# Kernel tuning notes

Measured on AMD Instinct MI355X. Metric: run time of the kernel, lower is better.

## Reference

```python
import jax, jax.numpy as jnp
import numpy as np

D_MODEL = 512
HEADS = 8
D_FF = 1024
EPS = 1e-5


def layer_norm(x, gamma, beta):
    mu = jnp.mean(x, axis=-1, keepdims=True)
    var = jnp.mean(jnp.square(x - mu), axis=-1, keepdims=True)
    return (x - mu) * jax.lax.rsqrt(var + EPS) * gamma + beta


def mha(q, k, v, mask=None):
    # q,k,v: [B, S, D]; no input/output projections in the original module
    B, Sq, D = q.shape
    Sk = k.shape[1]
    dk = D // HEADS
    qh = q.reshape(B, Sq, HEADS, dk).transpose(0, 2, 1, 3)  # [B,H,Sq,dk]
    kh = k.reshape(B, Sk, HEADS, dk).transpose(0, 2, 1, 3)
    vh = v.reshape(B, Sk, HEADS, dk).transpose(0, 2, 1, 3)
    scores = jnp.einsum('bhqd,bhkd->bhqk', qh, kh) / np.sqrt(dk).astype(q.dtype)
    if mask is not None:
        scores = jnp.where(mask == 0, jnp.asarray(-1e9, scores.dtype), scores)
    attn = jax.nn.softmax(scores, axis=-1)  # dropout is identity in eval mode
    out = jnp.einsum('bhqk,bhkd->bhqd', attn, vh)
    return out.transpose(0, 2, 1, 3).reshape(B, Sq, D)


def setup_inputs() -> dict:
    key = jax.random.key(0)
    ks = jax.random.split(key, 8)
    B, S = 4, 2048
    x = jax.random.normal(ks[0], (B, S, D_MODEL), dtype=jnp.float32)
    encoder_output = jax.random.normal(ks[1], (B, S, D_MODEL), dtype=jnp.float32)
    mask = jax.random.randint(ks[2], (B, 1, S, S), 0, 2, dtype=jnp.int32)
    params = {
        'ln1_g': jnp.ones((D_MODEL,), jnp.float32), 'ln1_b': jnp.zeros((D_MODEL,), jnp.float32),
        'ln2_g': jnp.ones((D_MODEL,), jnp.float32), 'ln2_b': jnp.zeros((D_MODEL,), jnp.float32),
        'ln3_g': jnp.ones((D_MODEL,), jnp.float32), 'ln3_b': jnp.zeros((D_MODEL,), jnp.float32),
        'W1': jax.random.normal(ks[3], (D_MODEL, D_FF), jnp.float32) * (1.0 / np.sqrt(D_MODEL)),
        'b1': jnp.zeros((D_FF,), jnp.float32),
        'W2': jax.random.normal(ks[4], (D_FF, D_MODEL), jnp.float32) * (1.0 / np.sqrt(D_FF)),
        'b2': jnp.zeros((D_MODEL,), jnp.float32),
    }
    return {'x': x, 'encoder_output': encoder_output, 'mask': mask, **params}


def reference(x, encoder_output, mask, ln1_g, ln1_b, ln2_g, ln2_b, ln3_g, ln3_b, W1, b1, W2, b2):
    # pre-norm masked self-attention + residual (dropout = identity, eval mode)
    x1 = layer_norm(x, ln1_g, ln1_b)
    x = x + mha(x1, x1, x1, mask)
    # pre-norm cross-attention + residual
    x1 = layer_norm(x, ln2_g, ln2_b)
    x = x + mha(x1, encoder_output, encoder_output, None)
    # pre-norm FFN + residual
    x1 = layer_norm(x, ln3_g, ln3_b)
    h = jax.nn.relu(x1 @ W1 + b1)
    x = x + (h @ W2 + b2)
    return x
```

## Files before the change

kernel.cpp:

```cpp
#include <hip/hip_runtime.h>
#include <hip/hip_bf16.h>

#define D_MODEL 512
#define HEADS   8
#define DK      64
#define D_FF    1024
#define SEQ     2048
#define BATCH   4
#define NTOK    (BATCH*SEQ)
#define NELEM   (NTOK*D_MODEL)

#define QSCALE  0.18033688011112042f
#define MFIX    40.0f

typedef __attribute__((ext_vector_type(8))) short bf8_t;
typedef __attribute__((ext_vector_type(4))) float f4_t;

#define GLD16(gp, lp) __builtin_amdgcn_global_load_lds( \
    (const __attribute__((address_space(1))) void*)(gp), \
    (__attribute__((address_space(3))) void*)(lp), 16, 0, 0)

__device__ __forceinline__ float ldf(const void* p, size_t i, int f32) {
    return f32 ? ((const float*)p)[i] : __bfloat162float(((const __hip_bfloat16*)p)[i]);
}
__device__ __forceinline__ short f2bf(float f) {
    union { __hip_bfloat16 h; short s; } u; u.h = __float2bfloat16(f); return u.s;
}
__device__ __forceinline__ float bf2f(short s) {
    return __uint_as_float(((unsigned)(unsigned short)s) << 16);
}
__device__ __forceinline__ unsigned fbits(float f) { return __float_as_uint(f); }

__device__ __forceinline__ float fast_exp2(float x) {
    float r; asm("v_exp_f32 %0, %1" : "=v"(r) : "v"(x)); return r;
}

__global__ void detect_k(const uint4* __restrict__ w, int* __restrict__ flags) {
    __shared__ int found;
    if (threadIdx.x == 0) found = 0;
    __syncthreads();
    int hit = 0;
    for (int i = threadIdx.x; i < 4096; i += 256) {
        uint4 u = w[i];
        if (((u.x & 0x7F80u) == 0x7F80u) || ((u.y & 0x7F80u) == 0x7F80u) ||
            ((u.z & 0x7F80u) == 0x7F80u) || ((u.w & 0x7F80u) == 0x7F80u)) hit = 1;
    }
    if (hit) atomicOr(&found, 1);
    __syncthreads();
    if (threadIdx.x == 0) flags[0] = found ? 1 : 0;
}

__device__ __forceinline__ void transpose_body(const void* src, __hip_bfloat16* dst,
                                               int K, int N, int bxi, int byi, int f32,
                                               __hip_bfloat16 (*t)[33]) {
    int bx = bxi * 32, by = byi * 32;
    int tx = threadIdx.x & 31, ty = threadIdx.x >> 5;
    #pragma unroll
    for (int j = 0; j < 32; j += 8)
        t[ty + j][tx] = __float2bfloat16(ldf(src, (size_t)(by + ty + j) * N + bx + tx, f32));
    __syncthreads();
    #pragma unroll
    for (int j = 0; j < 32; j += 8)
        dst[(size_t)(bx + ty + j) * K + by + tx] = t[tx][ty + j];
}

__global__ __launch_bounds__(256)
void prep_k(const void* __restrict__ enc, const int* __restrict__ mask,
            const void* __restrict__ W1, const void* __restrict__ W2,
            const void* __restrict__ x, const void* __restrict__ ln1g,
            const void* __restrict__ ln1b,
            const int* __restrict__ flagp,
            __hip_bfloat16* __restrict__ bufE, unsigned* __restrict__ mb,
            __hip_bfloat16* __restrict__ W1T, __hip_bfloat16* __restrict__ W2T,
            float* __restrict__ bufX, __hip_bfloat16* __restrict__ bufQ) {
    __shared__ __hip_bfloat16 t[32][33];
    int f32 = *flagp;
    int bid = blockIdx.x;
    if (bid < 16384) {
        int i = bid * 256 + threadIdx.x;
        bufE[i] = __float2bfloat16(ldf(enc, i, f32));
    } else if (bid < 18432) {
        int row  = (bid - 16384) * 4 + (threadIdx.x >> 6);
        int lane = threadIdx.x & 63;
        const int* mr = mask + (size_t)row * SEQ;
        for (int it = 0; it < SEQ/64; it++) {
            unsigned long long bal = __ballot(mr[it*64 + lane] != 0);
            if (lane == 0)  mb[(size_t)row*(SEQ/32) + it*2]     = (unsigned)bal;
            if (lane == 32) mb[(size_t)row*(SEQ/32) + it*2 + 1] = (unsigned)(bal >> 32);
        }
    } else if (bid < 18944) {
        int lb = bid - 18432;
        transpose_body(W1, W1T, D_MODEL, D_FF, lb & 31, lb >> 5, f32, t);
    } else if (bid < 19456) {
        int lb = bid - 18944;
        transpose_body(W2, W2T, D_FF, D_MODEL, lb & 15, lb >> 4, f32, t);
    } else {
        int row  = (bid - 19456) * 4 + (threadIdx.x >> 6);
        int lane = threadIdx.x & 63;
        size_t base = (size_t)row * D_MODEL;
        float v[8];
        float s = 0.f;
        #pragma unroll
        for (int i = 0; i < 8; i++) { v[i] = ldf(x, base + lane + i*64, f32); s += v[i]; }
        #pragma unroll
        for (int off = 32; off; off >>= 1) s += __shfl_xor(s, off);
        float mu = s * (1.f / D_MODEL);
        float ss = 0.f;
        #pragma unroll
        for (int i = 0; i < 8; i++) { float d = v[i] - mu; ss += d * d; }
        #pragma unroll
        for (int off = 32; off; off >>= 1) ss += __shfl_xor(ss, off);
        float rstd = rsqrtf(ss * (1.f / D_MODEL) + 1e-5f);
        #pragma unroll
        for (int i = 0; i < 8; i++) {
            int c = lane + i*64;
            bufX[base + c] = v[i];
            bufQ[base + c] = __float2bfloat16((v[i] - mu) * rstd * ldf(ln1g, c, f32) + ldf(ln1b, c, f32));
        }
    }
}

__global__ __launch_bounds__(256)
void layernorm_k(const float* __restrict__ x, const void* __restrict__ g,
                 const void* __restrict__ b, const int* __restrict__ flagp,
                 __hip_bfloat16* __restrict__ y) {
    int f32  = *flagp;
    int row  = blockIdx.x * 4 + (threadIdx.x >> 6);
    int lane = threadIdx.x & 63;
    const float* xr = x + (size_t)row * D_MODEL;
    float v[8];
    float s = 0.f;
    #pragma unroll
    for (int i = 0; i < 8; i++) { v[i] = xr[lane + i*64]; s += v[i]; }
    #pragma unroll
    for (int off = 32; off; off >>= 1) s += __shfl_xor(s, off);
    float mu = s * (1.f / D_MODEL);
    float ss = 0.f;
    #pragma unroll
    for (int i = 0; i < 8; i++) { float d = v[i] - mu; ss += d * d; }
    #pragma unroll
    for (int off = 32; off; off >>= 1) ss += __shfl_xor(ss, off);
    float rstd = rsqrtf(ss * (1.f / D_MODEL) + 1e-5f);
    __hip_bfloat16* yr = y + (size_t)row * D_MODEL;
    #pragma unroll
    for (int i = 0; i < 8; i++) {
        int c = lane + i*64;
        yr[c] = __float2bfloat16((v[i] - mu) * rstd * ldf(g, c, f32) + ldf(b, c, f32));
    }
}

__device__ __forceinline__ bf8_t prescale_q(bf8_t q) {
    bf8_t r;
    #pragma unroll
    for (int j = 0; j < 8; j++) r[j] = f2bf(bf2f(q[j]) * QSCALE);
    return r;
}

template<bool HAS_MASK>
__global__ __launch_bounds__(256, 2)
void attn_mfma_k(const __hip_bfloat16* __restrict__ Q, const __hip_bfloat16* __restrict__ K,
                 const __hip_bfloat16* __restrict__ V, const unsigned* __restrict__ mbits,
                 float* __restrict__ Xout) {
    int bid0 = blockIdx.x;
    int bid = ((bid0 & 7) << 6) | (bid0 >> 3);
    int qt = bid & 15;
    int h  = (bid >> 4) & 7;
    int b  = bid >> 7;
    int q0 = qt * 128;
    int tid  = threadIdx.x;
    int w    = tid >> 6;
    int lane = tid & 63;
    int c    = lane & 15;
    int quad = lane >> 4;

    __shared__ __hip_bfloat16 Kt[4][64 * 64];
    __shared__ __hip_bfloat16 VT[4][64 * 64];
    __shared__ __hip_bfloat16 Pb[4][2][16 * 64];

    bf8_t qf[2][2];
    #pragma unroll
    for (int g = 0; g < 2; g++) {
        const __hip_bfloat16* qrp = Q + ((size_t)(b*SEQ + q0 + 32*w + 16*g + c)) * D_MODEL + h*DK;
        qf[g][0] = prescale_q(*(const bf8_t*)(qrp + quad*8));
        qf[g][1] = prescale_q(*(const bf8_t*)(qrp + 32 + quad*8));
    }

    int kpo[4][2], vpo[4][2];
    #pragma unroll
    for (int t = 0; t < 4; t++)
        #pragma unroll
        for (int kh = 0; kh < 2; kh++) {
            int row = 16*t + c;
            kpo[t][kh] = (row*64 + (((4*kh + quad) ^ (row & 7)) * 8)) * 2;
            vpo[t][kh] = (row*64 + (((4*kh + quad) ^ (row & 7) ^ ((row >> 3) & 7)) * 8)) * 2;
        }

    int key0 = (tid >> 3) * 2, d0 = (tid & 7) * 8;
    int vtwo[8];
    #pragma unroll
    for (int j = 0; j < 8; j++) {
        int dk = d0 + j;
        int ch = (key0 >> 3) ^ (dk & 7) ^ ((dk >> 3) & 7);
        vtwo[j] = dk*128 + ch*16 + (key0 & 7)*2;
    }

    int krow[2], kc8[2];
    #pragma unroll
    for (int i = 0; i < 2; i++) {
        int idx = i*256 + tid;
        krow[i] = idx >> 3;
        kc8[i]  = ((idx & 7) ^ (krow[i] & 7)) * 8;
    }

    char* pbw[2] = { (char*)&Pb[w][0][0], (char*)&Pb[w][1][0] };
    int pwoff[4], proff[2];
    #pragma unroll
    for (int nt = 0; nt < 4; nt++)
        pwoff[nt] = c*128 + (((2*nt + (quad >> 1)) ^ (c & 7)) * 16) + (quad & 1)*8;
    #pragma unroll
    for (int kh = 0; kh < 2; kh++)
        proff[kh] = c*128 + (((4*kh + quad) ^ (c & 7)) * 16);

    const unsigned* mrp[2] = {nullptr, nullptr};
    if (HAS_MASK) {
        mrp[0] = mbits + (size_t)(b*SEQ + q0 + 32*w + c) * (SEQ/32);
        mrp[1] = mrp[0] + (size_t)16 * (SEQ/32);
    }
    int qsh = quad * 4;

    short onev = (c == 0) ? (short)0x3F80 : (short)0;
    bf8_t ones = {onev, onev, onev, onev, onev, onev, onev, onev};

    f4_t o[2][4];
    #pragma unroll
    for (int g = 0; g < 2; g++)
        #pragma unroll
        for (int mt = 0; mt < 4; mt++) o[g][mt] = (f4_t){0.f,0.f,0.f,0.f};
    f4_t l_acc[2] = {(f4_t){0.f,0.f,0.f,0.f}, (f4_t){0.f,0.f,0.f,0.f}};

    const size_t kvbase = (size_t)b * SEQ * D_MODEL + (size_t)h * DK;

    auto loadV = [&](int k0, bf8_t (&r0)[2], bf8_t (&r1)[2]) {
        #pragma unroll
        for (int t = 0; t < 2; t++) {
            const __hip_bfloat16* Vg = V + kvbase + (size_t)(k0 + t*64 + key0) * D_MODEL + d0;
            r0[t] = *(const bf8_t*)Vg;
            r1[t] = *(const bf8_t*)(Vg + D_MODEL);
        }
    };
    auto stageK = [&](int k0, int bufbase) {
        #pragma unroll
        for (int t = 0; t < 2; t++) {
            const __hip_bfloat16* Kg = K + kvbase + (size_t)(k0 + t*64) * D_MODEL;
            GLD16(Kg + (size_t)krow[0]*D_MODEL + kc8[0], (char*)&Kt[bufbase + t][0] + (w*64) * 16);
            GLD16(Kg + (size_t)krow[1]*D_MODEL + kc8[1], (char*)&Kt[bufbase + t][0] + (256 + w*64) * 16);
        }
    };
    auto writeV = [&](const bf8_t (&r0)[2], const bf8_t (&r1)[2], int bufbase) {
        #pragma unroll
        for (int t = 0; t < 2; t++) {
            const unsigned* v0u = (const unsigned*)&r0[t];
            const unsigned* v1u = (const unsigned*)&r1[t];
            char* vb = (char*)&VT[bufbase + t][0];
            #pragma unroll
            for (int dw = 0; dw < 4; dw++) {
                *(unsigned*)(vb + vtwo[2*dw])     = __builtin_amdgcn_perm(v1u[dw], v0u[dw], 0x05040100u);
                *(unsigned*)(vb + vtwo[2*dw + 1]) = __builtin_amdgcn_perm(v1u[dw], v0u[dw], 0x07060302u);
            }
        }
    };

    uint4 pm[2];
    if (HAS_MASK) { pm[0] = *(const uint4*)(mrp[0]); pm[1] = *(const uint4*)(mrp[1]); }
    bf8_t cv0[2], cv1[2];
    loadV(0, cv0, cv1);
    stageK(0, 0);
    writeV(cv0, cv1, 0);
    __syncthreads();

    for (int ph = 0; ph < SEQ/128; ph++) {
        int pb = (ph & 1) ? 2 : 0;
        int nb = pb ^ 2;

        uint4 nm[2];
        bf8_t nv0[2], nv1[2];
        if (ph < SEQ/128 - 1) {
            int kn = (ph + 1) * 128;
            if (HAS_MASK) {
                nm[0] = *(const uint4*)(mrp[0] + (kn >> 5));
                nm[1] = *(const uint4*)(mrp[1] + (kn >> 5));
            }
            loadV(kn, nv0, nv1);
            stageK(kn, nb);
        }

        #pragma unroll
        for (int t = 0; t < 2; t++) {
            const char* ktb = (const char*)&Kt[pb + t][0];
            const char* vtb = (const char*)&VT[pb + t][0];

            f4_t s[2][4];
            #pragma unroll
            for (int nt = 0; nt < 4; nt++) {
                s[0][nt] = (f4_t){-MFIX,-MFIX,-MFIX,-MFIX};
                s[1][nt] = (f4_t){-MFIX,-MFIX,-MFIX,-MFIX};
            }
            __builtin_amdgcn_s_setprio(1);
            #pragma unroll
            for (int nt = 0; nt < 4; nt++)
                #pragma unroll
                for (int kh = 0; kh < 2; kh++) {
                    bf8_t kf = *(const bf8_t*)(ktb + kpo[nt][kh]);
                    s[0][nt] = __builtin_amdgcn_mfma_f32_16x16x32_bf16(kf, qf[0][kh], s[0][nt], 0, 0, 0);
                    s[1][nt] = __builtin_amdgcn_mfma_f32_16x16x32_bf16(kf, qf[1][kh], s[1][nt], 0, 0, 0);
                }
            __builtin_amdgcn_s_setprio(0);

            #pragma unroll
            for (int g = 0; g < 2; g++) {
                unsigned wq0 = 0xffffffffu, wq1 = 0xffffffffu;
                if (HAS_MASK) {
                    wq0 = (t ? pm[g].z : pm[g].x) >> qsh;
                    wq1 = (t ? pm[g].w : pm[g].y) >> qsh;
                }
                #pragma unroll
                for (int nt = 0; nt < 4; nt++) {
                    #pragma unroll
                    for (int r = 0; r < 4; r++) {
                        float p = fast_exp2(s[g][nt][r]);
                        if (HAS_MASK) {
                            unsigned sel = (nt < 2) ? wq0 : wq1;
                            if (!((sel >> ((nt & 1)*16 + r)) & 1u)) p = 0.f;
                        }
                        s[g][nt][r] = p;
                    }
                    unsigned pk0 = __builtin_amdgcn_perm(fbits(s[g][nt][1]), fbits(s[g][nt][0]), 0x07060302u);
                    unsigned pk1 = __builtin_amdgcn_perm(fbits(s[g][nt][3]), fbits(s[g][nt][2]), 0x07060302u);
                    *(uint2*)(pbw[g] + pwoff[nt]) = make_uint2(pk0, pk1);
                }
            }

            __builtin_amdgcn_s_setprio(1);
            #pragma unroll
            for (int kh = 0; kh < 2; kh++) {
                bf8_t pfA = *(const bf8_t*)(pbw[0] + proff[kh]);
                bf8_t pfB = *(const bf8_t*)(pbw[1] + proff[kh]);
                l_acc[0] = __builtin_amdgcn_mfma_f32_16x16x32_bf16(ones, pfA, l_acc[0], 0, 0, 0);
                l_acc[1] = __builtin_amdgcn_mfma_f32_16x16x32_bf16(ones, pfB, l_acc[1], 0, 0, 0);
                #pragma unroll
                for (int mt = 0; mt < 4; mt++) {
                    bf8_t vf = *(const bf8_t*)(vtb + vpo[mt][kh]);
                    o[0][mt] = __builtin_amdgcn_mfma_f32_16x16x32_bf16(vf, pfA, o[0][mt], 0, 0, 0);
                    o[1][mt] = __builtin_amdgcn_mfma_f32_16x16x32_bf16(vf, pfB, o[1][mt], 0, 0, 0);
                }
            }
            __builtin_amdgcn_s_setprio(0);
        }

        if (ph < SEQ/128 - 1) {
            writeV(nv0, nv1, nb);
            if (HAS_MASK) { pm[0] = nm[0]; pm[1] = nm[1]; }
        }
        __syncthreads();
    }

    #pragma unroll
    for (int g = 0; g < 2; g++) {
        float lq = __shfl(l_acc[g][0], c);
        float il = 1.f / fmaxf(lq, 1e-35f);
        size_t rb = ((size_t)(b*SEQ + q0 + 32*w + 16*g + c)) * D_MODEL + h*DK;
        #pragma unroll
        for (int mt = 0; mt < 4; mt++) {
            float4* xp = (float4*)(Xout + rb + 16*mt + quad*4);
            float4 x4 = *xp;
            x4.x += o[g][mt][0] * il;
            x4.y += o[g][mt][1] * il;
            x4.z += o[g][mt][2] * il;
            x4.w += o[g][mt][3] * il;
            *xp = x4;
        }
    }
}

__global__ __launch_bounds__(256, 2)
void gemm_relu_k(const __hip_bfloat16* __restrict__ A, const __hip_bfloat16* __restrict__ BT,
                 const void* __restrict__ bias, const int* __restrict__ flagp,
                 __hip_bfloat16* __restrict__ C, int Ksz, int Nsz) {
    int f32 = *flagp;
    __shared__ __hip_bfloat16 As[2][128 * 64];
    __shared__ __hip_bfloat16 Bs[2][128 * 64];
    int tid  = threadIdx.x;
    int w    = tid >> 6;
    int c    = tid & 15;
    int quad = (tid >> 4) & 3;
    int wy = w >> 1, wx = w & 1;
    int lin = blockIdx.y * gridDim.x + blockIdx.x;
    int swz = ((lin & 7) << 6) | (lin >> 3);
    int r0 = (swz >> 3) * 128, c0 = (swz & 7) * 128;

    f4_t acc[4][4];
    #pragma unroll
    for (int i = 0; i < 4; i++)
        #pragma unroll
        for (int j = 0; j < 4; j++) acc[i][j] = (f4_t){0.f,0.f,0.f,0.f};

    auto stage = [&](int k0, int bi) {
        #pragma unroll
        for (int i = 0; i < 4; i++) {
            int idx = i*256 + tid;
            int row = idx >> 3, c8 = idx & 7;
            GLD16(A  + (size_t)(r0 + row) * Ksz + k0 + ((c8 ^ (row & 7)) * 8),
                  (char*)&As[bi][0] + (size_t)(i*256 + w*64) * 16);
            GLD16(BT + (size_t)(c0 + row) * Ksz + k0 + ((c8 ^ (row & 7)) * 8),
                  (char*)&Bs[bi][0] + (size_t)(i*256 + w*64) * 16);
        }
    };

    stage(0, 0);
    __syncthreads();
    int nk = Ksz >> 6;
    for (int ks = 0; ks < nk; ks++) {
        int bi = ks & 1;
        if (ks + 1 < nk) stage((ks + 1) << 6, bi ^ 1);

        #pragma unroll
        for (int kh = 0; kh < 2; kh++) {
            bf8_t af[4], bf[4];
            #pragma unroll
            for (int mt = 0; mt < 4; mt++) {
                int row = wy*64 + mt*16 + c;
                af[mt] = *(const bf8_t*)&As[bi][row*64 + (((kh*4 + quad) ^ (row & 7)) * 8)];
            }
            #pragma unroll
            for (int nt = 0; nt < 4; nt++) {
                int row = wx*64 + nt*16 + c;
                bf[nt] = *(const bf8_t*)&Bs[bi][row*64 + (((kh*4 + quad) ^ (row & 7)) * 8)];
            }
            #pragma unroll
            for (int mt = 0; mt < 4; mt++)
                #pragma unroll
                for (int nt = 0; nt < 4; nt++)
                    acc[mt][nt] = __builtin_amdgcn_mfma_f32_16x16x32_bf16(af[mt], bf[nt], acc[mt][nt], 0, 0, 0);
        }
        __syncthreads();
    }

    #pragma unroll
    for (int mt = 0; mt < 4; mt++)
        #pragma unroll
        for (int nt = 0; nt < 4; nt++) {
            int col = c0 + wx*64 + nt*16 + c;
            float bv = ldf(bias, col, f32);
            #pragma unroll
            for (int r = 0; r < 4; r++) {
                int m = r0 + wy*64 + mt*16 + quad*4 + r;
                C[(size_t)m * Nsz + col] = __float2bfloat16(fmaxf(acc[mt][nt][r] + bv, 0.f));
            }
        }
}

__global__ __launch_bounds__(256, 2)
void gemm_out_k(const __hip_bfloat16* __restrict__ A, const __hip_bfloat16* __restrict__ BT,
                const void* __restrict__ bias, const float* __restrict__ resid,
                const int* __restrict__ flagp, void* __restrict__ out, int Ksz, int Nsz) {
    int f32 = *flagp;
    __shared__ __hip_bfloat16 As[2][128 * 64];
    __shared__ __hip_bfloat16 Bs[2][64 * 64];
    int tid  = threadIdx.x;
    int w    = tid >> 6;
    int c    = tid & 15;
    int quad = (tid >> 4) & 3;
    int lin = blockIdx.y * gridDim.x + blockIdx.x;
    int swz = ((lin & 7) << 6) | (lin >> 3);
    int r0 = (swz >> 3) * 128, c0 = (swz & 7) * 64;

    f4_t acc[2][4];
    #pragma unroll
    for (int i = 0; i < 2; i++)
        #pragma unroll
        for (int j = 0; j < 4; j++) acc[i][j] = (f4_t){0.f,0.f,0.f,0.f};

    auto stage = [&](int k0, int bi) {
        #pragma unroll
        for (int i = 0; i < 4; i++) {
            int idx = i*256 + tid;
            int row = idx >> 3, c8 = idx & 7;
            GLD16(A + (size_t)(r0 + row) * Ksz + k0 + ((c8 ^ (row & 7)) * 8),
                  (char*)&As[bi][0] + (size_t)(i*256 + w*64) * 16);
        }
        #pragma unroll
        for (int i = 0; i < 2; i++) {
            int idx = i*256 + tid;
            int row = idx >> 3, c8 = idx & 7;
            GLD16(BT + (size_t)(c0 + row) * Ksz + k0 + ((c8 ^ (row & 7)) * 8),
                  (char*)&Bs[bi][0] + (size_t)(i*256 + w*64) * 16);
        }
    };

    stage(0, 0);
    __syncthreads();
    int nk = Ksz >> 6;
    for (int ks = 0; ks < nk; ks++) {
        int bi = ks & 1;
        if (ks + 1 < nk) stage((ks + 1) << 6, bi ^ 1);

        #pragma unroll
        for (int kh = 0; kh < 2; kh++) {
            bf8_t af[2], bf[4];
            #pragma unroll
            for (int mt = 0; mt < 2; mt++) {
                int row = w*32 + mt*16 + c;
                af[mt] = *(const bf8_t*)&As[bi][row*64 + (((kh*4 + quad) ^ (row & 7)) * 8)];
            }
            #pragma unroll
            for (int nt = 0; nt < 4; nt++) {
                int row = nt*16 + c;
                bf[nt] = *(const bf8_t*)&Bs[bi][row*64 + (((kh*4 + quad) ^ (row & 7)) * 8)];
            }
            #pragma unroll
            for (int mt = 0; mt < 2; mt++)
                #pragma unroll
                for (int nt = 0; nt < 4; nt++)
                    acc[mt][nt] = __builtin_amdgcn_mfma_f32_16x16x32_bf16(af[mt], bf[nt], acc[mt][nt], 0, 0, 0);
        }
        __syncthreads();
    }

    #pragma unroll
    for (int mt = 0; mt < 2; mt++)
        #pragma unroll
        for (int nt = 0; nt < 4; nt++) {
            int col = c0 + nt*16 + c;
            float bv = ldf(bias, col, f32);
            #pragma unroll
            for (int r = 0; r < 4; r++) {
                int m = r0 + w*32 + mt*16 + quad*4 + r;
                float v = acc[mt][nt][r] + bv + resid[(size_t)m * Nsz + col];
                if (f32) ((float*)out)[(size_t)m * Nsz + col] = v;
                else     ((__hip_bfloat16*)out)[(size_t)m * Nsz + col] = __float2bfloat16(v);
            }
        }
}

extern "C" void kernel_launch(void* const* d_in, const int* in_sizes, int n_in,
                              void* d_out, int out_size, void* d_ws, size_t ws_size,
                              hipStream_t stream) {
    const void* x    = d_in[0];
    const void* enc  = d_in[1];
    const int*  mask = (const int*)d_in[2];
    const void* ln1g = d_in[3];
    const void* ln1b = d_in[4];
    const void* ln2g = d_in[5];
    const void* ln2b = d_in[6];
    const void* ln3g = d_in[7];
    const void* ln3b = d_in[8];
    const void* W1   = d_in[9];
    const void* b1   = d_in[10];
    const void* W2   = d_in[11];
    const void* b2   = d_in[12];

    char* ws = (char*)d_ws;
    float*          bufX  = (float*)ws;
    __hip_bfloat16* bufQ  = (__hip_bfloat16*)(ws + (16u<<20));
    __hip_bfloat16* bufE  = (__hip_bfloat16*)(ws + (24u<<20));
    __hip_bfloat16* bufH  = (__hip_bfloat16*)(ws + (32u<<20));
    __hip_bfloat16* W1T   = (__hip_bfloat16*)(ws + (48u<<20));
    __hip_bfloat16* W2T   = (__hip_bfloat16*)(ws + (49u<<20));
    unsigned*       mbits = (unsigned*)(ws + (50u<<20));
    int*            flags = (int*)(ws + (52u<<20));

    dim3 blk(256);
    detect_k<<<1, blk, 0, stream>>>((const uint4*)x, flags);
    prep_k<<<21504, blk, 0, stream>>>(enc, mask, W1, W2, x, ln1g, ln1b, flags,
                                      bufE, mbits, W1T, W2T, bufX, bufQ);

    attn_mfma_k<true><<<BATCH*HEADS*(SEQ/128), blk, 0, stream>>>(bufQ, bufQ, bufQ, mbits, bufX);
    layernorm_k<<<NTOK/4, blk, 0, stream>>>(bufX, ln2g, ln2b, flags, bufQ);
    attn_mfma_k<false><<<BATCH*HEADS*(SEQ/128), blk, 0, stream>>>(bufQ, bufE, bufE, nullptr, bufX);
    layernorm_k<<<NTOK/4, blk, 0, stream>>>(bufX, ln3g, ln3b, flags, bufQ);
    gemm_relu_k<<<dim3(D_FF/128, NTOK/128), blk, 0, stream>>>(bufQ, W1T, b1, flags, bufH, D_MODEL, D_FF);
    gemm_out_k<<<dim3(D_MODEL/64, NTOK/128), blk, 0, stream>>>(bufH, W2T, b2, bufX, flags, d_out, D_FF, D_MODEL);
}
```

Baseline: 330.3 us.

## Vectorize prep and layernorm I/O, shrink attention K/V tiles for higher occupancy

The prep kernel's encoder bf16 conversion and the LN1 path now read and write 8 contiguous elements per thread with float4/bf8 vectors, cutting the block count. The layernorm kernel uses the same vectorized row layout. The attention kernel stages one 64-key tile per phase instead of two, halving its K/V shared memory so launch bounds can request 3 blocks per CU. The trade is twice as many loop iterations and barriers in attention, and possibly more register pressure under the tighter bound.

```diff
diff --git a/kernel.cpp b/kernel.cpp
--- a/kernel.cpp
+++ b/kernel.cpp
@@ -76,11 +76,20 @@
     __shared__ __hip_bfloat16 t[32][33];
     int f32 = *flagp;
     int bid = blockIdx.x;
-    if (bid < 16384) {
-        int i = bid * 256 + threadIdx.x;
-        bufE[i] = __float2bfloat16(ldf(enc, i, f32));
-    } else if (bid < 18432) {
-        int row  = (bid - 16384) * 4 + (threadIdx.x >> 6);
+    if (bid < 2048) {
+        size_t i0 = ((size_t)bid * 256 + threadIdx.x) * 8;
+        bf8_t o8;
+        if (f32) {
+            const float4* ep = (const float4*)((const float*)enc + i0);
+            float4 a = ep[0], b4 = ep[1];
+            o8[0]=f2bf(a.x);  o8[1]=f2bf(a.y);  o8[2]=f2bf(a.z);  o8[3]=f2bf(a.w);
+            o8[4]=f2bf(b4.x); o8[5]=f2bf(b4.y); o8[6]=f2bf(b4.z); o8[7]=f2bf(b4.w);
+        } else {
+            o8 = *(const bf8_t*)((const __hip_bfloat16*)enc + i0);
+        }
+        *(bf8_t*)(bufE + i0) = o8;
+    } else if (bid < 4096) {
+        int row  = (bid - 2048) * 4 + (threadIdx.x >> 6);
         int lane = threadIdx.x & 63;
         const int* mr = mask + (size_t)row * SEQ;
         for (int it = 0; it < SEQ/64; it++) {
@@ -88,20 +97,31 @@
             if (lane == 0)  mb[(size_t)row*(SEQ/32) + it*2]     = (unsigned)bal;
             if (lane == 32) mb[(size_t)row*(SEQ/32) + it*2 + 1] = (unsigned)(bal >> 32);
         }
-    } else if (bid < 18944) {
-        int lb = bid - 18432;
+    } else if (bid < 4608) {
+        int lb = bid - 4096;
         transpose_body(W1, W1T, D_MODEL, D_FF, lb & 31, lb >> 5, f32, t);
-    } else if (bid < 19456) {
-        int lb = bid - 18944;
+    } else if (bid < 5120) {
+        int lb = bid - 4608;
         transpose_body(W2, W2T, D_FF, D_MODEL, lb & 15, lb >> 4, f32, t);
     } else {
-        int row  = (bid - 19456) * 4 + (threadIdx.x >> 6);
+        int row  = (bid - 5120) * 4 + (threadIdx.x >> 6);
         int lane = threadIdx.x & 63;
+        int c0   = lane * 8;
         size_t base = (size_t)row * D_MODEL;
         float v[8];
+        if (f32) {
+            const float4* xp = (const float4*)((const float*)x + base + c0);
+            float4 a = xp[0], b4 = xp[1];
+            v[0]=a.x; v[1]=a.y; v[2]=a.z; v[3]=a.w;
+            v[4]=b4.x; v[5]=b4.y; v[6]=b4.z; v[7]=b4.w;
+        } else {
+            bf8_t x8 = *(const bf8_t*)((const __hip_bfloat16*)x + base + c0);
+            #pragma unroll
+            for (int j = 0; j < 8; j++) v[j] = bf2f(x8[j]);
+        }
         float s = 0.f;
         #pragma unroll
-        for (int i = 0; i < 8; i++) { v[i] = ldf(x, base + lane + i*64, f32); s += v[i]; }
+        for (int i = 0; i < 8; i++) s += v[i];
         #pragma unroll
         for (int off = 32; off; off >>= 1) s += __shfl_xor(s, off);
         float mu = s * (1.f / D_MODEL);
@@ -111,12 +131,13 @@
         #pragma unroll
         for (int off = 32; off; off >>= 1) ss += __shfl_xor(ss, off);
         float rstd = rsqrtf(ss * (1.f / D_MODEL) + 1e-5f);
-        #pragma unroll
-        for (int i = 0; i < 8; i++) {
-            int c = lane + i*64;
-            bufX[base + c] = v[i];
-            bufQ[base + c] = __float2bfloat16((v[i] - mu) * rstd * ldf(ln1g, c, f32) + ldf(ln1b, c, f32));
-        }
+        *(float4*)(bufX + base + c0)     = make_float4(v[0], v[1], v[2], v[3]);
+        *(float4*)(bufX + base + c0 + 4) = make_float4(v[4], v[5], v[6], v[7]);
+        bf8_t q8;
+        #pragma unroll
+        for (int j = 0; j < 8; j++)
+            q8[j] = f2bf((v[j] - mu) * rstd * ldf(ln1g, c0 + j, f32) + ldf(ln1b, c0 + j, f32));
+        *(bf8_t*)(bufQ + base + c0) = q8;
     }
 }
 
@@ -127,11 +148,14 @@
     int f32  = *flagp;
     int row  = blockIdx.x * 4 + (threadIdx.x >> 6);
     int lane = threadIdx.x & 63;
+    int c0   = lane * 8;
     const float* xr = x + (size_t)row * D_MODEL;
-    float v[8];
+    const float4* xp = (const float4*)(xr + c0);
+    float4 a = xp[0], b4 = xp[1];
+    float v[8] = {a.x, a.y, a.z, a.w, b4.x, b4.y, b4.z, b4.w};
     float s = 0.f;
     #pragma unroll
-    for (int i = 0; i < 8; i++) { v[i] = xr[lane + i*64]; s += v[i]; }
+    for (int i = 0; i < 8; i++) s += v[i];
     #pragma unroll
     for (int off = 32; off; off >>= 1) s += __shfl_xor(s, off);
     float mu = s * (1.f / D_MODEL);
@@ -141,12 +165,11 @@
     #pragma unroll
     for (int off = 32; off; off >>= 1) ss += __shfl_xor(ss, off);
     float rstd = rsqrtf(ss * (1.f / D_MODEL) + 1e-5f);
-    __hip_bfloat16* yr = y + (size_t)row * D_MODEL;
-    #pragma unroll
-    for (int i = 0; i < 8; i++) {
-        int c = lane + i*64;
-        yr[c] = __float2bfloat16((v[i] - mu) * rstd * ldf(g, c, f32) + ldf(b, c, f32));
-    }
+    bf8_t y8;
+    #pragma unroll
+    for (int j = 0; j < 8; j++)
+        y8[j] = f2bf((v[j] - mu) * rstd * ldf(g, c0 + j, f32) + ldf(b, c0 + j, f32));
+    *(bf8_t*)(y + (size_t)row * D_MODEL + c0) = y8;
 }
 
 __device__ __forceinline__ bf8_t prescale_q(bf8_t q) {
@@ -157,7 +180,7 @@
 }
 
 template<bool HAS_MASK>
-__global__ __launch_bounds__(256, 2)
+__global__ __launch_bounds__(256, 3)
 void attn_mfma_k(const __hip_bfloat16* __restrict__ Q, const __hip_bfloat16* __restrict__ K,
                  const __hip_bfloat16* __restrict__ V, const unsigned* __restrict__ mbits,
                  float* __restrict__ Xout) {
@@ -173,8 +196,8 @@
     int c    = lane & 15;
     int quad = lane >> 4;
 
-    __shared__ __hip_bfloat16 Kt[4][64 * 64];
-    __shared__ __hip_bfloat16 VT[4][64 * 64];
+    __shared__ __hip_bfloat16 Kt[2][64 * 64];
+    __shared__ __hip_bfloat16 VT[2][64 * 64];
     __shared__ __hip_bfloat16 Pb[4][2][16 * 64];
 
     bf8_t qf[2][2];
@@ -240,64 +263,54 @@
 
     const size_t kvbase = (size_t)b * SEQ * D_MODEL + (size_t)h * DK;
 
-    auto loadV = [&](int k0, bf8_t (&r0)[2], bf8_t (&r1)[2]) {
-        #pragma unroll
-        for (int t = 0; t < 2; t++) {
-            const __hip_bfloat16* Vg = V + kvbase + (size_t)(k0 + t*64 + key0) * D_MODEL + d0;
-            r0[t] = *(const bf8_t*)Vg;
-            r1[t] = *(const bf8_t*)(Vg + D_MODEL);
-        }
+    auto loadV = [&](int k0, bf8_t& r0, bf8_t& r1) {
+        const __hip_bfloat16* Vg = V + kvbase + (size_t)(k0 + key0) * D_MODEL + d0;
+        r0 = *(const bf8_t*)Vg;
+        r1 = *(const bf8_t*)(Vg + D_MODEL);
     };
-    auto stageK = [&](int k0, int bufbase) {
-        #pragma unroll
-        for (int t = 0; t < 2; t++) {
-            const __hip_bfloat16* Kg = K + kvbase + (size_t)(k0 + t*64) * D_MODEL;
-            GLD16(Kg + (size_t)krow[0]*D_MODEL + kc8[0], (char*)&Kt[bufbase + t][0] + (w*64) * 16);
-            GLD16(Kg + (size_t)krow[1]*D_MODEL + kc8[1], (char*)&Kt[bufbase + t][0] + (256 + w*64) * 16);
-        }
+    auto stageK = [&](int k0, int bi) {
+        const __hip_bfloat16* Kg = K + kvbase + (size_t)k0 * D_MODEL;
+        GLD16(Kg + (size_t)krow[0]*D_MODEL + kc8[0], (char*)&Kt[bi][0] + (w*64) * 16);
+        GLD16(Kg + (size_t)krow[1]*D_MODEL + kc8[1], (char*)&Kt[bi][0] + (256 + w*64) * 16);
     };
-    auto writeV = [&](const bf8_t (&r0)[2], const bf8_t (&r1)[2], int bufbase) {
-        #pragma unroll
-        for (int t = 0; t < 2; t++) {
-            const unsigned* v0u = (const unsigned*)&r0[t];
-            const unsigned* v1u = (const unsigned*)&r1[t];
-            char* vb = (char*)&VT[bufbase + t][0];
-            #pragma unroll
-            for (int dw = 0; dw < 4; dw++) {
-                *(unsigned*)(vb + vtwo[2*dw])     = __builtin_amdgcn_perm(v1u[dw], v0u[dw], 0x05040100u);
-                *(unsigned*)(vb + vtwo[2*dw + 1]) = __builtin_amdgcn_perm(v1u[dw], v0u[dw], 0x07060302u);
-            }
+    auto writeV = [&](const bf8_t& r0, const bf8_t& r1, int bi) {
+        const unsigned* v0u = (const unsigned*)&r0;
+        const unsigned* v1u = (const unsigned*)&r1;
+        char* vb = (char*)&VT[bi][0];
+        #pragma unroll
+        for (int dw = 0; dw < 4; dw++) {
+            *(unsigned*)(vb + vtwo[2*dw])     = __builtin_amdgcn_perm(v1u[dw], v0u[dw], 0x05040100u);
+            *(unsigned*)(vb + vtwo[2*dw + 1]) = __builtin_amdgcn_perm(v1u[dw], v0u[dw], 0x07060302u);
         }
     };
 
-    uint4 pm[2];
-    if (HAS_MASK) { pm[0] = *(const uint4*)(mrp[0]); pm[1] = *(const uint4*)(mrp[1]); }
-    bf8_t cv0[2], cv1[2];
+    uint2 pm[2];
+    if (HAS_MASK) { pm[0] = *(const uint2*)(mrp[0]); pm[1] = *(const uint2*)(mrp[1]); }
+    bf8_t cv0, cv1;
     loadV(0, cv0, cv1);
     stageK(0, 0);
     writeV(cv0, cv1, 0);
     __syncthreads();
 
-    for (int ph = 0; ph < SEQ/128; ph++) {
-        int pb = (ph & 1) ? 2 : 0;
-        int nb = pb ^ 2;
-
-        uint4 nm[2];
-        bf8_t nv0[2], nv1[2];
-        if (ph < SEQ/128 - 1) {
-            int kn = (ph + 1) * 128;
+    for (int ph = 0; ph < SEQ/64; ph++) {
+        int bi = ph & 1;
+        int ni = bi ^ 1;
+
+        uint2 nm[2];
+        bf8_t nv0, nv1;
+        if (ph < SEQ/64 - 1) {
+            int kn = (ph + 1) * 64;
             if (HAS_MASK) {
-                nm[0] = *(const uint4*)(mrp[0] + (kn >> 5));
-                nm[1] = *(const uint4*)(mrp[1] + (kn >> 5));
+                nm[0] = *(const uint2*)(mrp[0] + (kn >> 5));
+                nm[1] = *(const uint2*)(mrp[1] + (kn >> 5));
             }
             loadV(kn, nv0, nv1);
-            stageK(kn, nb);
-        }
-
-        #pragma unroll
-        for (int t = 0; t < 2; t++) {
-            const char* ktb = (const char*)&Kt[pb + t][0];
-            const char* vtb = (const char*)&VT[pb + t][0];
+            stageK(kn, ni);
+        }
+
+        {
+            const char* ktb = (const char*)&Kt[bi][0];
+            const char* vtb = (const char*)&VT[bi][0];
 
             f4_t s[2][4];
             #pragma unroll
@@ -320,8 +333,8 @@
             for (int g = 0; g < 2; g++) {
                 unsigned wq0 = 0xffffffffu, wq1 = 0xffffffffu;
                 if (HAS_MASK) {
-                    wq0 = (t ? pm[g].z : pm[g].x) >> qsh;
-                    wq1 = (t ? pm[g].w : pm[g].y) >> qsh;
+                    wq0 = pm[g].x >> qsh;
+                    wq1 = pm[g].y >> qsh;
                 }
                 #pragma unroll
                 for (int nt = 0; nt < 4; nt++) {
@@ -357,8 +370,8 @@
             __builtin_amdgcn_s_setprio(0);
         }
 
-        if (ph < SEQ/128 - 1) {
-            writeV(nv0, nv1, nb);
+        if (ph < SEQ/64 - 1) {
+            writeV(nv0, nv1, ni);
             if (HAS_MASK) { pm[0] = nm[0]; pm[1] = nm[1]; }
         }
         __syncthreads();
@@ -571,8 +584,8 @@
 
     dim3 blk(256);
     detect_k<<<1, blk, 0, stream>>>((const uint4*)x, flags);
-    prep_k<<<21504, blk, 0, stream>>>(enc, mask, W1, W2, x, ln1g, ln1b, flags,
-                                      bufE, mbits, W1T, W2T, bufX, bufQ);
+    prep_k<<<7168, blk, 0, stream>>>(enc, mask, W1, W2, x, ln1g, ln1b, flags,
+                                     bufE, mbits, W1T, W2T, bufX, bufQ);
 
     attn_mfma_k<true><<<BATCH*HEADS*(SEQ/128), blk, 0, stream>>>(bufQ, bufQ, bufQ, mbits, bufX);
     layernorm_k<<<NTOK/4, blk, 0, stream>>>(bufX, ln2g, ln2b, flags, bufQ);
```

After: 369.0 us. +11.7%, slower.
